# Performance work log

Hardware: AMD Instinct MI355X
Metric: run time of the kernel (lower is better)

Reference implementation:

```python
import jax, jax.numpy as jnp
import numpy as np
import math

NUM_HEADS = 16

def get_slopes(n):
    def pow2(n):
        start = 2 ** (-2 ** (-(math.log2(n) - 3)))
        return [start * start ** i for i in range(n)]
    if math.log2(n).is_integer():
        return pow2(n)
    c = 2 ** math.floor(math.log2(n))
    return pow2(c) + get_slopes(2 * c)[0::2][: n - c]


def setup_inputs() -> dict:
    key = jax.random.key(0)
    ks = jax.random.split(key, 5)
    B, T, C = 2, 2048, 1024
    return {
        "x": jax.random.normal(ks[0], (B, T, C), dtype=jnp.float32),
        "W_qkv": jax.random.normal(ks[1], (C, 3 * C), dtype=jnp.float32) * 0.02,
        "b_qkv": jax.random.normal(ks[2], (3 * C,), dtype=jnp.float32) * 0.02,
        "W_proj": jax.random.normal(ks[3], (C, C), dtype=jnp.float32) * 0.02,
        "b_proj": jax.random.normal(ks[4], (C,), dtype=jnp.float32) * 0.02,
    }


def reference(x, W_qkv, b_qkv, W_proj, b_proj):
    B, T, C = x.shape
    H = NUM_HEADS
    D = C // H
    qkv = x @ W_qkv + b_qkv                       # [B,T,3C]
    q, k, v = jnp.split(qkv, 3, axis=-1)
    q = q.reshape(B, T, H, D).transpose(0, 2, 1, 3)  # [B,H,T,D]
    k = k.reshape(B, T, H, D).transpose(0, 2, 1, 3)
    v = v.reshape(B, T, H, D).transpose(0, 2, 1, 3)

    slopes = jnp.asarray(get_slopes(H), dtype=jnp.float32)  # [H]
    idx = jnp.arange(T)
    # alibi_bias(L).T in source: -(i-j) for j<=i, 0 for j>i  == min(j-i, 0)
    alibi = jnp.minimum(idx[None, :] - idx[:, None], 0).astype(jnp.float32)  # [T,T]
    bias = slopes[:, None, None] * alibi          # [H,T,T]

    scale = 1.0 / math.sqrt(D)
    scores = jnp.einsum("bhtd,bhsd->bhts", q, k) * scale + bias[None]
    # NOTE: source code builds a causal -inf mask but never adds it -> non-causal
    w = jax.nn.softmax(scores, axis=-1)
    y = jnp.einsum("bhts,bhsd->bhtd", w, v)       # [B,H,T,D]
    y = y.transpose(0, 2, 1, 3).reshape(B, T, C)
    return y @ W_proj + b_proj
```

## Files before the change

### kernel.cpp

```cpp
#include <hip/hip_runtime.h>
#include <hip/hip_bf16.h>
#include <cmath>
#include <cstdint>

typedef __bf16 bf16_t;
typedef __bf16 bf16x8 __attribute__((ext_vector_type(8)));
typedef float f32x4 __attribute__((ext_vector_type(4)));
typedef float f32x8 __attribute__((ext_vector_type(8)));
typedef float f32x16 __attribute__((ext_vector_type(16)));
typedef unsigned int u32x2 __attribute__((ext_vector_type(2)));
typedef unsigned int u32x4 __attribute__((ext_vector_type(4)));

static_assert(sizeof(bf16x8) == 16, "bf16x8 must be 16B");

#define MFMA16(a, b, c) __builtin_amdgcn_mfma_f32_16x16x32_bf16((a), (b), (c), 0, 0, 0)
#define MFMA32(a, b, c) __builtin_amdgcn_mfma_f32_32x32x16_bf16((a), (b), (c), 0, 0, 0)

#define QSCALE 0.18033688011112042f

__device__ __forceinline__ void load_lds_16B(const bf16_t* gsrc, bf16_t* ldst) {
  __builtin_amdgcn_global_load_lds(
      (const __attribute__((address_space(1))) void*)gsrc,
      (__attribute__((address_space(3))) void*)ldst, 16, 0, 0);
}

__global__ void detect_dtype(const unsigned short* __restrict__ x,
                             int* __restrict__ flag) {
  const int lane = threadIdx.x;
  int cnt = 0;
#pragma unroll
  for (int t = 0; t < 8; ++t) {
    unsigned short u = x[2 * (lane + 64 * t)];
    int e = (u >> 7) & 0xFF;
    cnt += (e >= 90 && e <= 130) ? 1 : 0;
  }
#pragma unroll
  for (int off = 1; off < 64; off <<= 1) cnt += __shfl_xor(cnt, off, 64);
  if (lane == 0) *flag = (cnt < 300) ? 1 : 0;
}

__global__ __launch_bounds__(256) void convert_x(const void* __restrict__ x_,
                                                 bf16_t* __restrict__ xb,
                                                 const int* __restrict__ flagp) {
  const size_t idx = ((size_t)blockIdx.x * 256 + threadIdx.x) * 8;
  if (*flagp) {
    f32x8 v = *(const f32x8*)((const float*)x_ + idx);
    bf16x8 bv;
#pragma unroll
    for (int e = 0; e < 8; ++e) bv[e] = (bf16_t)v[e];
    *(bf16x8*)&xb[idx] = bv;
  } else {
    *(bf16x8*)&xb[idx] = *(const bf16x8*)((const bf16_t*)x_ + idx);
  }
}

__global__ __launch_bounds__(256) void wt_transpose(const void* __restrict__ W_,
                                                    bf16_t* __restrict__ Wt,
                                                    int K, int N,
                                                    const int* __restrict__ flagp) {
  __shared__ bf16_t tile[64 * 72];
  const int is_f32 = *flagp;
  const int tid = threadIdx.x;
  const int k0 = blockIdx.y * 64;
  const int n0 = blockIdx.x * 64;
  const int r = tid >> 3;
  const int c = (tid & 7) * 8;
#pragma unroll
  for (int t = 0; t < 2; ++t) {
    int rr = r + t * 32;
    if (is_f32) {
      const float* W = (const float*)W_;
      f32x8 v = *(const f32x8*)&W[(size_t)(k0 + rr) * N + n0 + c];
      bf16x8 bv;
#pragma unroll
      for (int e = 0; e < 8; ++e) bv[e] = (bf16_t)v[e];
      *(bf16x8*)&tile[rr * 72 + c] = bv;
    } else {
      const bf16_t* W = (const bf16_t*)W_;
      *(bf16x8*)&tile[rr * 72 + c] = *(const bf16x8*)&W[(size_t)(k0 + rr) * N + n0 + c];
    }
  }
  __syncthreads();
#pragma unroll
  for (int t = 0; t < 2; ++t) {
    int rr = r + t * 32;
    bf16x8 v;
#pragma unroll
    for (int e = 0; e < 8; ++e) v[e] = tile[(c + e) * 72 + rr];
    *(bf16x8*)&Wt[(size_t)(n0 + rr) * K + k0 + c] = v;
  }
}

__global__ __launch_bounds__(256, 3) void gemm_bt(
    const bf16_t* __restrict__ A, const bf16_t* __restrict__ Bt,
    const void* __restrict__ bias_, void* __restrict__ C_,
    bf16_t* __restrict__ qb, bf16_t* __restrict__ kb, bf16_t* __restrict__ vt,
    int M, int N, int K, int mode, const int* __restrict__ flagp) {
  __shared__ bf16_t As[128 * 64];
  __shared__ bf16_t Bs[128 * 64];
  const int is_f32 = *flagp;
  const int tid = threadIdx.x;
  const int wave = tid >> 6, lane = tid & 63;
  const int l16 = lane & 15, quad = lane >> 4;
  const int g = blockIdx.y * gridDim.x + blockIdx.x;
  const int q8 = (gridDim.x * gridDim.y) >> 3;
  const int ng = (g & 7) * q8 + (g >> 3);
  const int m0 = (ng / gridDim.x) * 128, n0 = (ng % gridDim.x) * 128;
  const int wm = (wave >> 1) * 64, wn = (wave & 1) * 64;
  const int lr = lane >> 3, lc = (lane & 7) * 8;
  f32x4 acc[4][4] = {};

  for (int k0 = 0; k0 < K; k0 += 64) {
#pragma unroll
    for (int t = 0; t < 4; ++t) {
      const int chunk = wave * 4 + t;
      const int row = chunk * 8 + lr;
      load_lds_16B(&A[(size_t)(m0 + row) * K + k0 + lc], &As[chunk * 512]);
      load_lds_16B(&Bt[(size_t)(n0 + row) * K + k0 + lc], &Bs[chunk * 512]);
    }
    __syncthreads();
#pragma unroll
    for (int ks = 0; ks < 2; ++ks) {
      bf16x8 af[4], bfr[4];
#pragma unroll
      for (int i = 0; i < 4; ++i) {
        af[i]  = *(const bf16x8*)&As[(wm + i * 16 + l16) * 64 + ks * 32 + quad * 8];
        bfr[i] = *(const bf16x8*)&Bs[(wn + i * 16 + l16) * 64 + ks * 32 + quad * 8];
      }
#pragma unroll
      for (int i = 0; i < 4; ++i)
#pragma unroll
        for (int j = 0; j < 4; ++j)
          acc[i][j] = MFMA16(af[i], bfr[j], acc[i][j]);
    }
    __syncthreads();
  }

#pragma unroll
  for (int j = 0; j < 4; ++j) {
    const int n = n0 + wn + j * 16 + l16;
    const float bv = is_f32 ? ((const float*)bias_)[n]
                            : (float)((const bf16_t*)bias_)[n];
    if (mode == 0) {
#pragma unroll
      for (int i = 0; i < 4; ++i)
#pragma unroll
        for (int r = 0; r < 4; ++r) {
          int m = m0 + wm + i * 16 + quad * 4 + r;
          float val = acc[i][j][r] + bv;
          if (is_f32) ((float*)C_)[(size_t)m * N + n] = val;
          else ((bf16_t*)C_)[(size_t)m * N + n] = (bf16_t)val;
        }
    } else {
      const int region = n >> 10;
      const int nn = n & 1023;
      const int hh = nn >> 6, dd = nn & 63;
      const float qs = (region == 0) ? QSCALE : 1.0f;
#pragma unroll
      for (int i = 0; i < 4; ++i)
#pragma unroll
        for (int r = 0; r < 4; ++r) {
          int m = m0 + wm + i * 16 + quad * 4 + r;
          int bb = m >> 11, tt = m & 2047;
          size_t bh = (size_t)(bb * 16 + hh);
          float val = (acc[i][j][r] + bv) * qs;
          if (region == 0)
            qb[(bh * 2048 + tt) * 64 + dd] = (bf16_t)val;
          else if (region == 1)
            kb[(bh * 2048 + tt) * 64 + dd] = (bf16_t)val;
          else
            vt[bh * 131072 + (size_t)dd * 2048 + tt] = (bf16_t)val;
        }
    }
  }
}

__global__ __launch_bounds__(256, 3) void gemm_bt64(
    const bf16_t* __restrict__ A, const bf16_t* __restrict__ Bt,
    const void* __restrict__ bias_, void* __restrict__ C_,
    int M, int N, int K, const int* __restrict__ flagp) {
  __shared__ bf16_t As[128 * 64];
  __shared__ bf16_t Bs[64 * 64];
  const int is_f32 = *flagp;
  const int tid = threadIdx.x;
  const int wave = tid >> 6, lane = tid & 63;
  const int l16 = lane & 15, quad = lane >> 4;
  const int g = blockIdx.y * gridDim.x + blockIdx.x;
  const int q8 = (gridDim.x * gridDim.y) >> 3;
  const int ng = (g & 7) * q8 + (g >> 3);
  const int m0 = (ng / gridDim.x) * 128, n0 = (ng % gridDim.x) * 64;
  const int wm = wave * 32;
  const int lr = lane >> 3, lc = (lane & 7) * 8;
  f32x4 acc[2][4] = {};

  for (int k0 = 0; k0 < K; k0 += 64) {
#pragma unroll
    for (int t = 0; t < 4; ++t) {
      const int chunk = wave * 4 + t;
      const int row = chunk * 8 + lr;
      load_lds_16B(&A[(size_t)(m0 + row) * K + k0 + lc], &As[chunk * 512]);
    }
#pragma unroll
    for (int t = 0; t < 2; ++t) {
      const int chunk = wave * 2 + t;
      const int row = chunk * 8 + lr;
      load_lds_16B(&Bt[(size_t)(n0 + row) * K + k0 + lc], &Bs[chunk * 512]);
    }
    __syncthreads();
#pragma unroll
    for (int ks = 0; ks < 2; ++ks) {
      bf16x8 af[2], bfr[4];
#pragma unroll
      for (int i = 0; i < 2; ++i)
        af[i] = *(const bf16x8*)&As[(wm + i * 16 + l16) * 64 + ks * 32 + quad * 8];
#pragma unroll
      for (int j = 0; j < 4; ++j)
        bfr[j] = *(const bf16x8*)&Bs[(j * 16 + l16) * 64 + ks * 32 + quad * 8];
#pragma unroll
      for (int i = 0; i < 2; ++i)
#pragma unroll
        for (int j = 0; j < 4; ++j)
          acc[i][j] = MFMA16(af[i], bfr[j], acc[i][j]);
    }
    __syncthreads();
  }

#pragma unroll
  for (int j = 0; j < 4; ++j) {
    const int n = n0 + j * 16 + l16;
    const float bv = is_f32 ? ((const float*)bias_)[n]
                            : (float)((const bf16_t*)bias_)[n];
#pragma unroll
    for (int i = 0; i < 2; ++i)
#pragma unroll
      for (int r = 0; r < 4; ++r) {
        int m = m0 + wm + i * 16 + quad * 4 + r;
        float val = acc[i][j][r] + bv;
        if (is_f32) ((float*)C_)[(size_t)m * N + n] = val;
        else ((bf16_t*)C_)[(size_t)m * N + n] = (bf16_t)val;
      }
  }
}

__global__ __launch_bounds__(512, 4) void attn_kernel(
    const bf16_t* __restrict__ qbuf, const bf16_t* __restrict__ kbuf,
    const bf16_t* __restrict__ vT, bf16_t* __restrict__ y) {
  const int T = 2048;
  __shared__ __align__(16) char smem[65536];
  bf16_t* KsA = (bf16_t*)smem;
  bf16_t* VsA = (bf16_t*)(smem + 32768);

  const int tid = threadIdx.x;
  const int wave = tid >> 6, lane = tid & 63;
  const int g2 = wave >> 2, wp = wave & 3;
  const int l32 = lane & 31, hi = lane >> 5;
  const int x7 = l32 & 7;
  const int d = blockIdx.y * 16 + blockIdx.x;
  const int slot = d >> 3;
  const int bh = (d & 7) * 4 + (slot >> 4);
  const int bx = slot & 15;
  const int b = bh >> 4, h = bh & 15;
  const int i0 = bx * 128 + wp * 32;
  const float L2E = 1.44269504088896f;
  const float c2 = exp2f(-0.5f * (float)(h + 1)) * L2E;

  bf16x8 qf[4];
  {
    const bf16_t* qrow = qbuf + ((size_t)bh * T + i0 + l32) * 64 + hi * 8;
#pragma unroll
    for (int kk = 0; kk < 4; ++kk) qf[kk] = *(const bf16x8*)&qrow[kk * 16];
  }

  f32x16 o[2] = {};
  float rsum = 0.f;

  const bf16_t* kbase = kbuf + (size_t)bh * T * 64;
  const bf16_t* vbase = vT + (size_t)bh * 64 * T;
  bf16_t* Kg = KsA + g2 * 8192;
  bf16_t* Vg = VsA + g2 * 8192;

  const int jbase = g2 * 1024;
  const float dif = (float)(4 * hi - i0 - l32);

  const int lr8 = lane >> 3;
  const int swz = ((lane & 7) ^ lr8) * 8;
  const bf16_t* kl0 = kbase + (size_t)(jbase + wp * 16 + lr8) * 64 + swz;
  const bf16_t* kl1 = kl0 + 8 * 64;
  const bf16_t* vl0 = vbase + (size_t)(wp * 16 + lr8) * T + jbase + swz;
  const bf16_t* vl1 = vl0 + (size_t)8 * T;
  bf16_t* kd0 = Kg + wp * 1024;
  bf16_t* vd0 = Vg + wp * 1024;

#define STAGE(bufsel, trel)                                         \
  do {                                                              \
    const size_t ko_ = (size_t)(trel) * 4096;                       \
    const size_t vo_ = (size_t)(trel) * 64;                         \
    bf16_t* kd_ = kd0 + (bufsel) * 4096;                            \
    bf16_t* vd_ = vd0 + (bufsel) * 4096;                            \
    load_lds_16B(kl0 + ko_, kd_);                                   \
    load_lds_16B(kl1 + ko_, kd_ + 512);                             \
    load_lds_16B(vl0 + vo_, vd_);                                   \
    load_lds_16B(vl1 + vo_, vd_ + 512);                             \
  } while (0)

  STAGE(0, 0);
  __asm__ volatile("s_waitcnt vmcnt(0)" ::: "memory");
  __syncthreads();

  for (int t = 0; t < 16; ++t) {
    const int cur = t & 1;
    const int j0 = jbase + t * 64;

    if (t < 15) STAGE(cur ^ 1, t + 1);

    const bf16_t* myKs = Kg + cur * 4096;
    const bf16_t* myVs = Vg + cur * 4096;

#pragma unroll
    for (int hl = 0; hl < 2; ++hl) {
      const int jblk = j0 + hl * 32;
      bf16x8 kf[4];
#pragma unroll
      for (int kk = 0; kk < 4; ++kk) {
        const int R = hl * 32 + l32;
        kf[kk] = *(const bf16x8*)&myKs[R * 64 + (((kk << 1) + hi) ^ x7) * 8];
      }
      f32x16 s = {};
      __builtin_amdgcn_s_setprio(1);
#pragma unroll
      for (int kk = 0; kk < 4; ++kk) s = MFMA32(kf[kk], qf[kk], s);
      __builtin_amdgcn_s_setprio(0);

      float rs = 0.f;
      if (jblk >= i0 + 31) {
#pragma unroll
        for (int r = 0; r < 16; ++r) {
          float p = exp2f(s[r]);
          rs += p; s[r] = p;
        }
      } else {
        const float cjb = c2 * ((float)jblk + dif);
        if (jblk + 31 <= i0) {
#pragma unroll
          for (int r = 0; r < 16; ++r) {
            const float kr = (float)((r & 3) + 8 * (r >> 2));
            float p = exp2f(fmaf(c2, kr, s[r] + cjb));
            rs += p; s[r] = p;
          }
        } else {
#pragma unroll
          for (int r = 0; r < 16; ++r) {
            const float kr = (float)((r & 3) + 8 * (r >> 2));
            float p = exp2f(s[r] + fminf(fmaf(c2, kr, cjb), 0.f));
            rs += p; s[r] = p;
          }
        }
      }
      rsum += rs;

      unsigned int w[8];
#pragma unroll
      for (int q = 0; q < 8; ++q)
        asm("v_cvt_pk_bf16_f32 %0, %1, %2"
            : "=v"(w[q]) : "v"(s[2 * q]), "v"(s[2 * q + 1]));
      u32x2 q02 = __builtin_amdgcn_permlane32_swap(w[0], w[2], false, false);
      u32x2 q13 = __builtin_amdgcn_permlane32_swap(w[1], w[3], false, false);
      u32x2 q46 = __builtin_amdgcn_permlane32_swap(w[4], w[6], false, false);
      u32x2 q57 = __builtin_amdgcn_permlane32_swap(w[5], w[7], false, false);
      u32x4 a0u = {q02[0], q13[0], q02[1], q13[1]};
      u32x4 a1u = {q46[0], q57[0], q46[1], q57[1]};
      bf16x8 af0 = __builtin_bit_cast(bf16x8, a0u);
      bf16x8 af1 = __builtin_bit_cast(bf16x8, a1u);

      bf16x8 vf[4];
#pragma unroll
      for (int db = 0; db < 2; ++db) {
        const int D = db * 32 + l32;
        vf[db * 2]     = *(const bf16x8*)&myVs[D * 64 + ((hl * 4 + hi) ^ x7) * 8];
        vf[db * 2 + 1] = *(const bf16x8*)&myVs[D * 64 + ((hl * 4 + 2 + hi) ^ x7) * 8];
      }
      __builtin_amdgcn_s_setprio(1);
#pragma unroll
      for (int db = 0; db < 2; ++db) {
        o[db] = MFMA32(af0, vf[db * 2], o[db]);
        o[db] = MFMA32(af1, vf[db * 2 + 1], o[db]);
      }
      __builtin_amdgcn_s_setprio(0);
    }

    __asm__ volatile("s_waitcnt vmcnt(0)" ::: "memory");
    __syncthreads();
  }
#undef STAGE

  rsum += __shfl_xor(rsum, 32, 64);

  float* exO = (float*)smem;
  float* exR = (float*)(smem + 33280);
  if (g2 == 1) {
    float* myO = exO + wp * (32 * 65);
#pragma unroll
    for (int db = 0; db < 2; ++db)
#pragma unroll
      for (int r = 0; r < 16; ++r) {
        const int row = (r & 3) + 8 * (r >> 2) + 4 * hi;
        myO[row * 65 + db * 32 + l32] = o[db][r];
      }
    if (lane < 32) exR[wp * 32 + lane] = rsum;
  }
  __syncthreads();
  if (g2 == 0) {
    float* myO = exO + wp * (32 * 65);
#pragma unroll
    for (int r = 0; r < 16; ++r) {
      const int row = (r & 3) + 8 * (r >> 2) + 4 * hi;
      const float denom = __shfl(rsum, row, 64) + exR[wp * 32 + row];
      const float rden = 1.0f / denom;
      const int ig = i0 + row;
#pragma unroll
      for (int db = 0; db < 2; ++db) {
        const float val = (o[db][r] + myO[row * 65 + db * 32 + l32]) * rden;
        y[((size_t)(b * 2048 + ig)) * 1024 + h * 64 + db * 32 + l32] = (bf16_t)val;
      }
    }
  }
}

extern "C" void kernel_launch(void* const* d_in, const int* in_sizes, int n_in,
                              void* d_out, int out_size, void* d_ws, size_t ws_size,
                              hipStream_t stream) {
  const void* x     = d_in[0];
  const void* Wqkv  = d_in[1];
  const void* bqkv  = d_in[2];
  const void* Wproj = d_in[3];
  const void* bproj = d_in[4];

  const size_t SEG = (size_t)32 * 2048 * 64;
  bf16_t* ws = (bf16_t*)d_ws;
  bf16_t* qb = ws;
  bf16_t* kb = ws + SEG;
  bf16_t* vt = ws + 2 * SEG;
  bf16_t* yb = ws + 3 * SEG;
  bf16_t* WqkvT  = yb;
  bf16_t* WprojT = qb;
  bf16_t* xb = (bf16_t*)d_out;
  int* flag1 = (int*)((char*)d_ws + (size_t)31 * 1024 * 1024);
  int* flag2 = (int*)((char*)d_ws + (size_t)4 * 1024 * 1024);

  detect_dtype<<<1, 64, 0, stream>>>((const unsigned short*)x, flag1);
  wt_transpose<<<dim3(48, 16), 256, 0, stream>>>(Wqkv, WqkvT, 1024, 3072, flag1);
  convert_x<<<2048, 256, 0, stream>>>(x, xb, flag1);
  gemm_bt<<<dim3(24, 32), 256, 0, stream>>>(xb, WqkvT, bqkv, nullptr, qb, kb, vt,
                                            4096, 3072, 1024, 1, flag1);
  attn_kernel<<<dim3(16, 32), 512, 0, stream>>>(qb, kb, vt, yb);
  detect_dtype<<<1, 64, 0, stream>>>((const unsigned short*)x, flag2);
  wt_transpose<<<dim3(16, 16), 256, 0, stream>>>(Wproj, WprojT, 1024, 1024, flag2);
  gemm_bt64<<<dim3(16, 32), 256, 0, stream>>>(yb, WprojT, bproj, d_out,
                                              4096, 1024, 1024, flag2);
}
```

Measured before the change: 216.3 us.

## Single-buffer V in attention LDS and fold dtype detection into kernels

The attention kernel now keeps only one V tile in LDS instead of two, shrinking shared memory from 64KB to 48KB so more blocks can fit per CU. To make that safe it reorders the waits and barriers: the next V tile loads only after the PV MFMAs finish, while K stays double-buffered. The separate detect_dtype launches are removed; each kernel now re-derives the dtype flag inline from a probe of x, saving two launches at the cost of redundant probe reads in every block. The diagonal-band exponent is also factored into a precomputed per-row exp2 multiplier, and the row sums are split across four accumulators to shorten dependency chains.

```diff
diff --git a/kernel.cpp b/kernel.cpp
--- a/kernel.cpp
+++ b/kernel.cpp
@@ -24,9 +24,8 @@
       (__attribute__((address_space(3))) void*)ldst, 16, 0, 0);
 }
 
-__global__ void detect_dtype(const unsigned short* __restrict__ x,
-                             int* __restrict__ flag) {
-  const int lane = threadIdx.x;
+__device__ __forceinline__ int detect_f32(const unsigned short* __restrict__ x) {
+  const int lane = threadIdx.x & 63;
   int cnt = 0;
 #pragma unroll
   for (int t = 0; t < 8; ++t) {
@@ -36,14 +35,14 @@
   }
 #pragma unroll
   for (int off = 1; off < 64; off <<= 1) cnt += __shfl_xor(cnt, off, 64);
-  if (lane == 0) *flag = (cnt < 300) ? 1 : 0;
+  return (cnt < 300) ? 1 : 0;
 }
 
 __global__ __launch_bounds__(256) void convert_x(const void* __restrict__ x_,
-                                                 bf16_t* __restrict__ xb,
-                                                 const int* __restrict__ flagp) {
+                                                 bf16_t* __restrict__ xb) {
+  const int is_f32 = detect_f32((const unsigned short*)x_);
   const size_t idx = ((size_t)blockIdx.x * 256 + threadIdx.x) * 8;
-  if (*flagp) {
+  if (is_f32) {
     f32x8 v = *(const f32x8*)((const float*)x_ + idx);
     bf16x8 bv;
 #pragma unroll
@@ -57,9 +56,9 @@
 __global__ __launch_bounds__(256) void wt_transpose(const void* __restrict__ W_,
                                                     bf16_t* __restrict__ Wt,
                                                     int K, int N,
-                                                    const int* __restrict__ flagp) {
+                                                    const unsigned short* __restrict__ xprobe) {
   __shared__ bf16_t tile[64 * 72];
-  const int is_f32 = *flagp;
+  const int is_f32 = detect_f32(xprobe);
   const int tid = threadIdx.x;
   const int k0 = blockIdx.y * 64;
   const int n0 = blockIdx.x * 64;
@@ -95,10 +94,10 @@
     const bf16_t* __restrict__ A, const bf16_t* __restrict__ Bt,
     const void* __restrict__ bias_, void* __restrict__ C_,
     bf16_t* __restrict__ qb, bf16_t* __restrict__ kb, bf16_t* __restrict__ vt,
-    int M, int N, int K, int mode, const int* __restrict__ flagp) {
+    int M, int N, int K, int mode, const unsigned short* __restrict__ xprobe) {
   __shared__ bf16_t As[128 * 64];
   __shared__ bf16_t Bs[128 * 64];
-  const int is_f32 = *flagp;
+  const int is_f32 = detect_f32(xprobe);
   const int tid = threadIdx.x;
   const int wave = tid >> 6, lane = tid & 63;
   const int l16 = lane & 15, quad = lane >> 4;
@@ -178,10 +177,10 @@
 __global__ __launch_bounds__(256, 3) void gemm_bt64(
     const bf16_t* __restrict__ A, const bf16_t* __restrict__ Bt,
     const void* __restrict__ bias_, void* __restrict__ C_,
-    int M, int N, int K, const int* __restrict__ flagp) {
+    int M, int N, int K, const unsigned short* __restrict__ xprobe) {
   __shared__ bf16_t As[128 * 64];
   __shared__ bf16_t Bs[64 * 64];
-  const int is_f32 = *flagp;
+  const int is_f32 = detect_f32(xprobe);
   const int tid = threadIdx.x;
   const int wave = tid >> 6, lane = tid & 63;
   const int l16 = lane & 15, quad = lane >> 4;
@@ -246,7 +245,7 @@
     const bf16_t* __restrict__ qbuf, const bf16_t* __restrict__ kbuf,
     const bf16_t* __restrict__ vT, bf16_t* __restrict__ y) {
   const int T = 2048;
-  __shared__ __align__(16) char smem[65536];
+  __shared__ __align__(16) char smem[49152];
   bf16_t* KsA = (bf16_t*)smem;
   bf16_t* VsA = (bf16_t*)(smem + 32768);
 
@@ -264,6 +263,11 @@
   const float L2E = 1.44269504088896f;
   const float c2 = exp2f(-0.5f * (float)(h + 1)) * L2E;
 
+  float er[16];
+#pragma unroll
+  for (int r = 0; r < 16; ++r)
+    er[r] = exp2f(c2 * (float)((r & 3) + 8 * (r >> 2)));
+
   bf16x8 qf[4];
   {
     const bf16_t* qrow = qbuf + ((size_t)bh * T + i0 + l32) * 64 + hi * 8;
@@ -277,7 +281,7 @@
   const bf16_t* kbase = kbuf + (size_t)bh * T * 64;
   const bf16_t* vbase = vT + (size_t)bh * 64 * T;
   bf16_t* Kg = KsA + g2 * 8192;
-  bf16_t* Vg = VsA + g2 * 8192;
+  bf16_t* Vg = VsA + g2 * 4096;
 
   const int jbase = g2 * 1024;
   const float dif = (float)(4 * hi - i0 - l32);
@@ -291,19 +295,22 @@
   bf16_t* kd0 = Kg + wp * 1024;
   bf16_t* vd0 = Vg + wp * 1024;
 
-#define STAGE(bufsel, trel)                                         \
+#define STAGE_K(bufsel, trel)                                       \
   do {                                                              \
     const size_t ko_ = (size_t)(trel) * 4096;                       \
-    const size_t vo_ = (size_t)(trel) * 64;                         \
     bf16_t* kd_ = kd0 + (bufsel) * 4096;                            \
-    bf16_t* vd_ = vd0 + (bufsel) * 4096;                            \
     load_lds_16B(kl0 + ko_, kd_);                                   \
     load_lds_16B(kl1 + ko_, kd_ + 512);                             \
-    load_lds_16B(vl0 + vo_, vd_);                                   \
-    load_lds_16B(vl1 + vo_, vd_ + 512);                             \
   } while (0)
-
-  STAGE(0, 0);
+#define STAGE_V(trel)                                               \
+  do {                                                              \
+    const size_t vo_ = (size_t)(trel) * 64;                         \
+    load_lds_16B(vl0 + vo_, vd0);                                   \
+    load_lds_16B(vl1 + vo_, vd0 + 512);                             \
+  } while (0)
+
+  STAGE_K(0, 0);
+  STAGE_V(0);
   __asm__ volatile("s_waitcnt vmcnt(0)" ::: "memory");
   __syncthreads();
 
@@ -311,10 +318,9 @@
     const int cur = t & 1;
     const int j0 = jbase + t * 64;
 
-    if (t < 15) STAGE(cur ^ 1, t + 1);
+    if (t < 15) STAGE_K(cur ^ 1, t + 1);
 
     const bf16_t* myKs = Kg + cur * 4096;
-    const bf16_t* myVs = Vg + cur * 4096;
 
 #pragma unroll
     for (int hl = 0; hl < 2; ++hl) {
@@ -331,32 +337,37 @@
       for (int kk = 0; kk < 4; ++kk) s = MFMA32(kf[kk], qf[kk], s);
       __builtin_amdgcn_s_setprio(0);
 
-      float rs = 0.f;
+      float rs0 = 0.f, rs1 = 0.f, rs2 = 0.f, rs3 = 0.f;
       if (jblk >= i0 + 31) {
 #pragma unroll
         for (int r = 0; r < 16; ++r) {
           float p = exp2f(s[r]);
-          rs += p; s[r] = p;
+          if ((r & 3) == 0) rs0 += p; else if ((r & 3) == 1) rs1 += p;
+          else if ((r & 3) == 2) rs2 += p; else rs3 += p;
+          s[r] = p;
         }
       } else {
         const float cjb = c2 * ((float)jblk + dif);
         if (jblk + 31 <= i0) {
 #pragma unroll
           for (int r = 0; r < 16; ++r) {
-            const float kr = (float)((r & 3) + 8 * (r >> 2));
-            float p = exp2f(fmaf(c2, kr, s[r] + cjb));
-            rs += p; s[r] = p;
+            float p = exp2f(s[r] + cjb) * er[r];
+            if ((r & 3) == 0) rs0 += p; else if ((r & 3) == 1) rs1 += p;
+            else if ((r & 3) == 2) rs2 += p; else rs3 += p;
+            s[r] = p;
           }
         } else {
 #pragma unroll
           for (int r = 0; r < 16; ++r) {
             const float kr = (float)((r & 3) + 8 * (r >> 2));
             float p = exp2f(s[r] + fminf(fmaf(c2, kr, cjb), 0.f));
-            rs += p; s[r] = p;
+            if ((r & 3) == 0) rs0 += p; else if ((r & 3) == 1) rs1 += p;
+            else if ((r & 3) == 2) rs2 += p; else rs3 += p;
+            s[r] = p;
           }
         }
       }
-      rsum += rs;
+      rsum += (rs0 + rs1) + (rs2 + rs3);
 
       unsigned int w[8];
 #pragma unroll
@@ -372,12 +383,18 @@
       bf16x8 af0 = __builtin_bit_cast(bf16x8, a0u);
       bf16x8 af1 = __builtin_bit_cast(bf16x8, a1u);
 
+      if (hl == 0) {
+        if (t < 15) __asm__ volatile("s_waitcnt vmcnt(2)" ::: "memory");
+        else        __asm__ volatile("s_waitcnt vmcnt(0)" ::: "memory");
+        __syncthreads();
+      }
+
       bf16x8 vf[4];
 #pragma unroll
       for (int db = 0; db < 2; ++db) {
         const int D = db * 32 + l32;
-        vf[db * 2]     = *(const bf16x8*)&myVs[D * 64 + ((hl * 4 + hi) ^ x7) * 8];
-        vf[db * 2 + 1] = *(const bf16x8*)&myVs[D * 64 + ((hl * 4 + 2 + hi) ^ x7) * 8];
+        vf[db * 2]     = *(const bf16x8*)&Vg[D * 64 + ((hl * 4 + hi) ^ x7) * 8];
+        vf[db * 2 + 1] = *(const bf16x8*)&Vg[D * 64 + ((hl * 4 + 2 + hi) ^ x7) * 8];
       }
       __builtin_amdgcn_s_setprio(1);
 #pragma unroll
@@ -388,10 +405,17 @@
       __builtin_amdgcn_s_setprio(0);
     }
 
-    __asm__ volatile("s_waitcnt vmcnt(0)" ::: "memory");
-    __syncthreads();
-  }
-#undef STAGE
+    __syncthreads();
+    if (t < 15) {
+      STAGE_V(t + 1);
+      __asm__ volatile("s_waitcnt vmcnt(2)" ::: "memory");
+    } else {
+      __asm__ volatile("s_waitcnt vmcnt(0)" ::: "memory");
+    }
+    __syncthreads();
+  }
+#undef STAGE_K
+#undef STAGE_V
 
   rsum += __shfl_xor(rsum, 32, 64);
 
@@ -434,6 +458,7 @@
   const void* bqkv  = d_in[2];
   const void* Wproj = d_in[3];
   const void* bproj = d_in[4];
+  const unsigned short* xprobe = (const unsigned short*)x;
 
   const size_t SEG = (size_t)32 * 2048 * 64;
   bf16_t* ws = (bf16_t*)d_ws;
@@ -444,17 +469,13 @@
   bf16_t* WqkvT  = yb;
   bf16_t* WprojT = qb;
   bf16_t* xb = (bf16_t*)d_out;
-  int* flag1 = (int*)((char*)d_ws + (size_t)31 * 1024 * 1024);
-  int* flag2 = (int*)((char*)d_ws + (size_t)4 * 1024 * 1024);
-
-  detect_dtype<<<1, 64, 0, stream>>>((const unsigned short*)x, flag1);
-  wt_transpose<<<dim3(48, 16), 256, 0, stream>>>(Wqkv, WqkvT, 1024, 3072, flag1);
-  convert_x<<<2048, 256, 0, stream>>>(x, xb, flag1);
+
+  wt_transpose<<<dim3(48, 16), 256, 0, stream>>>(Wqkv, WqkvT, 1024, 3072, xprobe);
+  convert_x<<<2048, 256, 0, stream>>>(x, xb);
   gemm_bt<<<dim3(24, 32), 256, 0, stream>>>(xb, WqkvT, bqkv, nullptr, qb, kb, vt,
-                                            4096, 3072, 1024, 1, flag1);
+                                            4096, 3072, 1024, 1, xprobe);
   attn_kernel<<<dim3(16, 32), 512, 0, stream>>>(qb, kb, vt, yb);
-  detect_dtype<<<1, 64, 0, stream>>>((const unsigned short*)x, flag2);
-  wt_transpose<<<dim3(16, 16), 256, 0, stream>>>(Wproj, WprojT, 1024, 1024, flag2);
+  wt_transpose<<<dim3(16, 16), 256, 0, stream>>>(Wproj, WprojT, 1024, 1024, xprobe);
   gemm_bt64<<<dim3(16, 32), 256, 0, stream>>>(yb, WprojT, bproj, d_out,
-                                              4096, 1024, 1024, flag2);
-}
+                                              4096, 1024, 1024, xprobe);
+}
```

Measured after the change: 224.3 us. 3.7% more time.
